# Kernel optimization log

Measured on AMD Instinct MI355X. Metric: run time of the kernel, lower is better.

Reference implementation:

```python
import jax, jax.numpy as jnp
import numpy as np

DIM = 96
NUM_HEADS = 3
WIN = 7  # window_size (square)


def _relative_position_index(wh, ww):
    coords = np.stack(np.meshgrid(np.arange(wh), np.arange(ww), indexing='ij'))  # [2, wh, ww]
    flat = coords.reshape(2, -1)  # [2, n]
    rel = flat[:, :, None] - flat[:, None, :]  # [2, n, n]
    rel = rel.transpose(1, 2, 0).astype(np.int64)
    rel[..., 0] += wh - 1
    rel[..., 1] += ww - 1
    rel[..., 0] *= 2 * ww - 1
    return rel.sum(-1)  # [n, n]


def setup_inputs() -> dict:
    key = jax.random.key(0)
    ks = jax.random.split(key, 9)
    b, n, c = 8192, WIN * WIN, DIM
    std = 0.02
    inp = {
        'x': jax.random.normal(ks[0], (b, n, c), jnp.float32),
        'v': jax.random.normal(ks[1], (b, n, c), jnp.float32),
        'w_q': jax.random.normal(ks[2], (c, c), jnp.float32) * std,
        'b_q': jnp.zeros((c,), jnp.float32),
        'w_kv': jax.random.normal(ks[3], (c, 2 * c), jnp.float32) * std,
        'b_kv': jnp.zeros((2 * c,), jnp.float32),
        'w_proj': jax.random.normal(ks[4], (c, c), jnp.float32) * std,
        'b_proj': jnp.zeros((c,), jnp.float32),
        'rpb_table': jax.random.normal(ks[5], ((2 * WIN - 1) * (2 * WIN - 1), NUM_HEADS), jnp.float32) * std,
        'rel_index': jnp.asarray(_relative_position_index(WIN, WIN), jnp.int32),
    }
    return inp


def reference(x, v, w_q, b_q, w_kv, b_kv, w_proj, b_proj, rpb_table, rel_index):
    b, n, c = x.shape
    h = NUM_HEADS
    hd = c // h
    scale = hd ** -0.5
    # q: [b, h, n, hd]
    q = (x @ w_q + b_q).reshape(b, n, h, hd).transpose(0, 2, 1, 3) * scale
    kv = (v @ w_kv + b_kv).reshape(b, n, 2, h, hd)
    k = kv[:, :, 0].transpose(0, 2, 1, 3)  # [b, h, n, hd]
    vv = kv[:, :, 1].transpose(0, 2, 1, 3)
    attn = jnp.einsum('bhqd,bhkd->bhqk', q, k)  # [b, h, n, n]
    bias = rpb_table[rel_index.reshape(-1)].reshape(n, n, h).transpose(2, 0, 1)  # [h, n, n]
    attn = jax.nn.softmax(attn + bias[None], axis=-1)
    out = jnp.einsum('bhqk,bhkd->bhqd', attn, vv).transpose(0, 2, 1, 3).reshape(b, n, c)
    return out @ w_proj + b_proj
```

## Files before the change

kernel.cpp:

```cpp
#include <hip/hip_runtime.h>
#include <hip/hip_bf16.h>

typedef __bf16 bf16x8 __attribute__((ext_vector_type(8)));
typedef float f32x4 __attribute__((ext_vector_type(4)));
typedef short s16x8 __attribute__((ext_vector_type(8)));
typedef short s16x4 __attribute__((ext_vector_type(4)));

#define NTOK 49
#define CDIM 96
#define KS_S 104
#define VT_S 56
#define BN_S 136
#define LOG2E 1.4426950408889634f

#if __has_builtin(__builtin_amdgcn_exp2f)
#define EXP2F(x) __builtin_amdgcn_exp2f(x)
#else
#define EXP2F(x) exp2f(x)
#endif

#define DRAIN() do { asm volatile("s_waitcnt lgkmcnt(0)" ::: "memory"); \
                     __builtin_amdgcn_sched_barrier(0); } while (0)

__device__ __forceinline__ unsigned short f2bf(float f) {
  __hip_bfloat16 h = __float2bfloat16(f);
  return __builtin_bit_cast(unsigned short, h);
}

__device__ __forceinline__ bf16x8 ld_cvt8(const float* p) {
  float4 a = *(const float4*)p;
  float4 b = *(const float4*)(p + 4);
  s16x8 r;
  r[0] = (short)f2bf(a.x); r[1] = (short)f2bf(a.y);
  r[2] = (short)f2bf(a.z); r[3] = (short)f2bf(a.w);
  r[4] = (short)f2bf(b.x); r[5] = (short)f2bf(b.y);
  r[6] = (short)f2bf(b.z); r[7] = (short)f2bf(b.w);
  return __builtin_bit_cast(bf16x8, r);
}

__global__ void prep(const float* __restrict__ wq, const float* __restrict__ wkv,
                     const float* __restrict__ wproj, const float* __restrict__ rpb,
                     const int* __restrict__ relidx, unsigned short* __restrict__ wsT,
                     float* __restrict__ biasf) {
  const int total = 36864 + 3 * 49 * 64;
  for (int i = blockIdx.x * 256 + threadIdx.x; i < total; i += gridDim.x * 256) {
    if (i < 9216) {
      int oc = i / 96, ic = i - oc * 96;
      wsT[i] = f2bf(wq[ic * 96 + oc]);
    } else if (i < 27648) {
      int j = i - 9216; int oc = j / 96, ic = j - oc * 96;
      wsT[i] = f2bf(wkv[ic * 192 + oc]);
    } else if (i < 36864) {
      int j = i - 27648; int oc = j / 96, ic = j - oc * 96;
      wsT[i] = f2bf(wproj[ic * 96 + oc]);
    } else {
      int j = i - 36864; int h = j / 3136; int rc = j - h * 3136;
      int r = rc >> 6, c = rc & 63;
      biasf[j] = (c < 49) ? rpb[relidx[r * 49 + c] * 3 + h] * LOG2E : 0.f;
    }
  }
}

__launch_bounds__(256, 4)
__global__ void attn_fused(const float* __restrict__ xg, const float* __restrict__ vg,
                           const float* __restrict__ bq, const float* __restrict__ bkv,
                           const float* __restrict__ bproj,
                           const unsigned short* __restrict__ wsT,
                           const float* __restrict__ biasf,
                           float* __restrict__ outg) {
  __shared__ __align__(16) unsigned char smem[38352];
  unsigned short* Ks  = (unsigned short*)smem;
  unsigned short* VVT = (unsigned short*)(smem + 10192);

  const int tid = threadIdx.x;
  const int lane = tid & 63;
  const int wv = tid >> 6;
  const int c16 = lane & 15;
  const int g4 = lane >> 4;
  const int win = blockIdx.x;
  const int q0 = (wv == 0) ? 0 : (wv == 1) ? 16 : (wv == 2) ? 32 : 33;
  unsigned short* bnc = (unsigned short*)(smem + 20944) + wv * (16 * BN_S);

  const int mp = wv & 1;
  const bool isK = (wv < 2);
  const int m0 = mp ? 32 : 0;
  const int m1 = mp ? 33 : 16;

  const float* base = xg + (size_t)win * (NTOK * CDIM);
  const float* vbase = vg + (size_t)win * (NTOK * CDIM);
  const float* xrow = base + (q0 + c16) * CDIM;
  const float* vrow0 = vbase + (m0 + c16) * CDIM;
  const float* vrow1 = vbase + (m1 + c16) * CDIM;

  bf16x8 xf[3], vf0[3], vf1[3];
#pragma unroll
  for (int k = 0; k < 3; ++k) {
    xf[k]  = ld_cvt8(xrow  + k * 32 + g4 * 8);
    vf0[k] = ld_cvt8(vrow0 + k * 32 + g4 * 8);
    vf1[k] = ld_cvt8(vrow1 + k * 32 + g4 * 8);
  }

  const float scale = 0.2550348742f;
#pragma unroll
  for (int nt = 0; nt < 6; ++nt) {
    f32x4 acc = {0, 0, 0, 0};
    const int ocl = nt * 16 + c16;
#pragma unroll
    for (int k = 0; k < 3; ++k) {
      bf16x8 b = *(const bf16x8*)(wsT + ocl * 96 + k * 32 + g4 * 8);
      acc = __builtin_amdgcn_mfma_f32_16x16x32_bf16(xf[k], b, acc, 0, 0, 0);
    }
    float bias = bq[ocl];
#pragma unroll
    for (int r = 0; r < 4; ++r)
      bnc[(4 * g4 + r) * BN_S + ocl] = f2bf((acc[r] + bias) * scale);
  }

#pragma unroll
  for (int nt = 0; nt < 6; ++nt) {
    const int ocl = (isK ? 0 : 96) + nt * 16 + c16;
    f32x4 a0 = {0, 0, 0, 0}, a1 = {0, 0, 0, 0};
#pragma unroll
    for (int k = 0; k < 3; ++k) {
      bf16x8 b = *(const bf16x8*)(wsT + 9216 + ocl * 96 + k * 32 + g4 * 8);
      a0 = __builtin_amdgcn_mfma_f32_16x16x32_bf16(vf0[k], b, a0, 0, 0, 0);
      a1 = __builtin_amdgcn_mfma_f32_16x16x32_bf16(vf1[k], b, a1, 0, 0, 0);
    }
    float bias = bkv[ocl];
    if (isK) {
#pragma unroll
      for (int r = 0; r < 4; ++r)
        Ks[(m0 + 4 * g4 + r) * KS_S + ocl] = f2bf(a0[r] + bias);
#pragma unroll
      for (int r = 0; r < 4; ++r)
        Ks[(m1 + 4 * g4 + r) * KS_S + ocl] = f2bf(a1[r] + bias);
    } else {
      int dim = ocl - 96;
      s16x4 p0;
#pragma unroll
      for (int r = 0; r < 4; ++r) p0[r] = (short)f2bf(a0[r] + bias);
      *(s16x4*)(VVT + dim * VT_S + (m0 + 4 * g4)) = p0;
      if (mp == 0) {
        s16x4 p1;
#pragma unroll
        for (int r = 0; r < 4; ++r) p1[r] = (short)f2bf(a1[r] + bias);
        *(s16x4*)(VVT + dim * VT_S + (16 + 4 * g4)) = p1;
      } else {
#pragma unroll
        for (int r = 0; r < 4; ++r)
          VVT[dim * VT_S + 33 + 4 * g4 + r] = f2bf(a1[r] + bias);
      }
    }
  }
  __syncthreads();

  const int q = q0 + c16;

  s16x8 vmask;
#pragma unroll
  for (int j = 0; j < 8; ++j)
    vmask[j] = (short)(((32 + g4 * 8 + j) < 49) ? 0xFFFF : 0x0000);

  f32x4 oacc[6] = {{0,0,0,0},{0,0,0,0},{0,0,0,0},{0,0,0,0},{0,0,0,0},{0,0,0,0}};

  auto softmax_pw = [&](const f32x4* s, const f32x4* bv, int pcol) {
    float vals[16];
#pragma unroll
    for (int kt = 0; kt < 4; ++kt)
#pragma unroll
      for (int r = 0; r < 4; ++r) {
        int key = 16 * kt + 4 * g4 + r;
        vals[kt * 4 + r] = (kt < 3 || key < 49) ? (s[kt][r] + bv[kt][r]) : -1e30f;
      }
    float m8[8];
#pragma unroll
    for (int j = 0; j < 8; ++j) m8[j] = fmaxf(vals[j], vals[j + 8]);
    float ma = fmaxf(m8[0], m8[4]), mb = fmaxf(m8[1], m8[5]);
    float mc = fmaxf(m8[2], m8[6]), md = fmaxf(m8[3], m8[7]);
    float mx = fmaxf(fmaxf(ma, mb), fmaxf(mc, md));
    mx = fmaxf(mx, __shfl_xor(mx, 16, 64));
    mx = fmaxf(mx, __shfl_xor(mx, 32, 64));
    float e[16];
#pragma unroll
    for (int j = 0; j < 16; ++j) e[j] = EXP2F(vals[j] - mx);
    float s8[8];
#pragma unroll
    for (int j = 0; j < 8; ++j) s8[j] = e[j] + e[j + 8];
    float sa = s8[0] + s8[4], sb = s8[1] + s8[5], sc = s8[2] + s8[6], sd = s8[3] + s8[7];
    float sum = (sa + sb) + (sc + sd);
    sum += __shfl_xor(sum, 16, 64);
    sum += __shfl_xor(sum, 32, 64);
    float rinv = 1.0f / sum;
#pragma unroll
    for (int kt = 0; kt < 4; ++kt) {
      s16x4 p;
#pragma unroll
      for (int r = 0; r < 4; ++r) p[r] = (short)f2bf(e[kt * 4 + r] * rinv);
      *(s16x4*)(bnc + c16 * BN_S + pcol + 16 * kt + 4 * g4) = p;
    }
  };

  auto pv_out = [&](int h, int pcol, int ocol) {
    bf16x8 ap0 = *(const bf16x8*)(bnc + c16 * BN_S + pcol + g4 * 8);
    bf16x8 ap1 = *(const bf16x8*)(bnc + c16 * BN_S + pcol + 32 + g4 * 8);
#pragma unroll
    for (int dt = 0; dt < 2; ++dt) {
      int dim = h * 32 + dt * 16 + c16;
      bf16x8 bv0 = *(const bf16x8*)(VVT + dim * VT_S + g4 * 8);
      s16x8 b1 = *(const s16x8*)(VVT + dim * VT_S + 32 + g4 * 8);
      b1 &= vmask;
      f32x4 o = __builtin_amdgcn_mfma_f32_16x16x32_bf16(ap0, bv0, (f32x4){0,0,0,0}, 0, 0, 0);
      o = __builtin_amdgcn_mfma_f32_16x16x32_bf16(ap1, __builtin_bit_cast(bf16x8, b1), o, 0, 0, 0);
#pragma unroll
      for (int r = 0; r < 4; ++r)
        bnc[(4 * g4 + r) * BN_S + ocol + dt * 16 + c16] = f2bf(o[r]);
    }
  };

  auto oproj = [&](int h, int ocol) {
    bf16x8 bo = *(const bf16x8*)(bnc + c16 * BN_S + ocol + g4 * 8);
#pragma unroll
    for (int mt = 0; mt < 6; ++mt) {
      bf16x8 a = *(const bf16x8*)(wsT + 27648 + (mt * 16 + c16) * 96 + h * 32 + g4 * 8);
      oacc[mt] = __builtin_amdgcn_mfma_f32_16x16x32_bf16(a, bo, oacc[mt], 0, 0, 0);
    }
  };

  f32x4 b0v[4], b1v[4];
  {
    const float* br0 = biasf + q * 64 + 4 * g4;
    const float* br1 = biasf + (49 + q) * 64 + 4 * g4;
#pragma unroll
    for (int kt = 0; kt < 4; ++kt) {
      b0v[kt] = *(const f32x4*)(br0 + 16 * kt);
      b1v[kt] = *(const f32x4*)(br1 + 16 * kt);
    }
  }
  bf16x8 qf0 = *(const bf16x8*)(bnc + c16 * BN_S + g4 * 8);
  bf16x8 qf1 = *(const bf16x8*)(bnc + c16 * BN_S + 32 + g4 * 8);
  bf16x8 qf2 = *(const bf16x8*)(bnc + c16 * BN_S + 64 + g4 * 8);

  f32x4 s0[4], s1[4];
#pragma unroll
  for (int kt = 0; kt < 4; ++kt) {
    bf16x8 ak = *(const bf16x8*)(Ks + (16 * kt + c16) * KS_S + g4 * 8);
    s0[kt] = __builtin_amdgcn_mfma_f32_16x16x32_bf16(ak, qf0, (f32x4){0,0,0,0}, 0, 0, 0);
  }
#pragma unroll
  for (int kt = 0; kt < 4; ++kt) {
    bf16x8 ak = *(const bf16x8*)(Ks + (16 * kt + c16) * KS_S + 32 + g4 * 8);
    s1[kt] = __builtin_amdgcn_mfma_f32_16x16x32_bf16(ak, qf1, (f32x4){0,0,0,0}, 0, 0, 0);
  }
  softmax_pw(s0, b0v, 0);
  softmax_pw(s1, b1v, 64);

  f32x4 b2v[4];
  {
    const float* br2 = biasf + (98 + q) * 64 + 4 * g4;
#pragma unroll
    for (int kt = 0; kt < 4; ++kt) b2v[kt] = *(const f32x4*)(br2 + 16 * kt);
  }
  f32x4 s2[4];
#pragma unroll
  for (int kt = 0; kt < 4; ++kt) {
    bf16x8 ak = *(const bf16x8*)(Ks + (16 * kt + c16) * KS_S + 64 + g4 * 8);
    s2[kt] = __builtin_amdgcn_mfma_f32_16x16x32_bf16(ak, qf2, (f32x4){0,0,0,0}, 0, 0, 0);
  }

  DRAIN();
  pv_out(0, 0, 0);
  pv_out(1, 64, 32);
  softmax_pw(s2, b2v, 64);

  DRAIN();
  oproj(0, 0);
  oproj(1, 32);
  pv_out(2, 64, 96);

  DRAIN();
  oproj(2, 96);

  {
    const bool store_ok = (wv < 3) || (c16 == 15);
    float* orow = outg + (size_t)win * (NTOK * CDIM) + q * 96;
#pragma unroll
    for (int mt = 0; mt < 6; ++mt) {
      int oc0 = mt * 16 + g4 * 4;
      if (store_ok) {
        float4 bb = *(const float4*)(bproj + oc0);
        float4 o4;
        o4.x = oacc[mt][0] + bb.x; o4.y = oacc[mt][1] + bb.y;
        o4.z = oacc[mt][2] + bb.z; o4.w = oacc[mt][3] + bb.w;
        *(float4*)(orow + oc0) = o4;
      }
    }
  }
}

extern "C" void kernel_launch(void* const* d_in, const int* in_sizes, int n_in,
                              void* d_out, int out_size, void* d_ws, size_t ws_size,
                              hipStream_t stream) {
  const float* x     = (const float*)d_in[0];
  const float* v     = (const float*)d_in[1];
  const float* wq    = (const float*)d_in[2];
  const float* bq    = (const float*)d_in[3];
  const float* wkv   = (const float*)d_in[4];
  const float* bkv   = (const float*)d_in[5];
  const float* wproj = (const float*)d_in[6];
  const float* bproj = (const float*)d_in[7];
  const float* rpb   = (const float*)d_in[8];
  const int*   relidx= (const int*)d_in[9];
  float* out = (float*)d_out;
  unsigned short* wsT = (unsigned short*)d_ws;
  float* biasf = (float*)((char*)d_ws + 73728);
  int nwin = in_sizes[0] / (NTOK * CDIM);

  hipLaunchKernelGGL(prep, dim3(181), dim3(256), 0, stream,
                     wq, wkv, wproj, rpb, relidx, wsT, biasf);
  hipLaunchKernelGGL(attn_fused, dim3(nwin), dim3(256), 0, stream,
                     x, v, bq, bkv, bproj, wsT, biasf, out);
}
```

Measured before the change: 251.0 us.

## Split fused attention into K/V projection kernel and attention kernel via workspace

Adds a proj_kv kernel that computes K and transposed V in bf16 and writes them to a global workspace. A second kernel, attn2, computes Q and then reads K and V^T straight from global memory to do softmax, PV and the output projection. Both new kernels use far less shared memory and declare 8 blocks per CU, and attn2 needs no block-wide barrier. The aim is higher occupancy and better latency hiding, paid for with about 165 MB of extra global write and read traffic. The old fused kernel remains as a fallback when the workspace is too small.

```diff
diff --git a/kernel.cpp b/kernel.cpp
--- a/kernel.cpp
+++ b/kernel.cpp
@@ -11,7 +11,12 @@
 #define KS_S 104
 #define VT_S 56
 #define BN_S 136
+#define PB_S 104
 #define LOG2E 1.4426950408889634f
+
+#define WS_K_B 111616
+#define WS_VT_B 77181952
+#define WS_NEED 165262400ull
 
 #if __has_builtin(__builtin_amdgcn_exp2f)
 #define EXP2F(x) __builtin_amdgcn_exp2f(x)
@@ -61,6 +66,254 @@
   }
 }
 
+__launch_bounds__(256, 8)
+__global__ void proj_kv(const float* __restrict__ vg, const float* __restrict__ bkv,
+                        const unsigned short* __restrict__ wsT,
+                        unsigned short* __restrict__ kbuf,
+                        unsigned short* __restrict__ vtbuf) {
+  __shared__ __align__(16) unsigned short bnc_all[4 * 16 * PB_S];
+  const int tid = threadIdx.x, lane = tid & 63, wv = tid >> 6;
+  const int c16 = lane & 15, g4 = lane >> 4;
+  const int win = blockIdx.x;
+  const int q0 = (wv == 0) ? 0 : (wv == 1) ? 16 : (wv == 2) ? 32 : 33;
+  unsigned short* bnc = bnc_all + wv * (16 * PB_S);
+
+  const float* vrow = vg + (size_t)win * (NTOK * CDIM) + (q0 + c16) * CDIM;
+  bf16x8 vf[3];
+#pragma unroll
+  for (int k = 0; k < 3; ++k) vf[k] = ld_cvt8(vrow + k * 32 + g4 * 8);
+
+#pragma unroll
+  for (int nt = 0; nt < 6; ++nt) {
+    const int ocl = 96 + nt * 16 + c16;
+    f32x4 acc = {0, 0, 0, 0};
+#pragma unroll
+    for (int k = 0; k < 3; ++k) {
+      bf16x8 b = *(const bf16x8*)(wsT + 9216 + ocl * 96 + k * 32 + g4 * 8);
+      acc = __builtin_amdgcn_mfma_f32_16x16x32_bf16(vf[k], b, acc, 0, 0, 0);
+    }
+    float bias = bkv[ocl];
+    const int dim = nt * 16 + c16;
+    const int rb = q0 + 4 * g4;
+    unsigned short* vtr = vtbuf + ((size_t)win * CDIM + dim) * VT_S;
+    if (wv < 3) {
+      s16x4 p;
+#pragma unroll
+      for (int r = 0; r < 4; ++r) p[r] = (short)f2bf(acc[r] + bias);
+      *(s16x4*)(vtr + rb) = p;
+    } else {
+#pragma unroll
+      for (int r = 0; r < 4; ++r) vtr[rb + r] = f2bf(acc[r] + bias);
+    }
+  }
+
+#pragma unroll
+  for (int nt = 0; nt < 6; ++nt) {
+    const int ocl = nt * 16 + c16;
+    f32x4 acc = {0, 0, 0, 0};
+#pragma unroll
+    for (int k = 0; k < 3; ++k) {
+      bf16x8 b = *(const bf16x8*)(wsT + 9216 + ocl * 96 + k * 32 + g4 * 8);
+      acc = __builtin_amdgcn_mfma_f32_16x16x32_bf16(vf[k], b, acc, 0, 0, 0);
+    }
+    float bias = bkv[ocl];
+#pragma unroll
+    for (int r = 0; r < 4; ++r)
+      bnc[(4 * g4 + r) * PB_S + ocl] = f2bf(acc[r] + bias);
+  }
+  DRAIN();
+  const bool store_ok = (wv < 3) || (c16 == 15);
+  if (store_ok) {
+    unsigned short* krow = kbuf + ((size_t)win * NTOK + q0 + c16) * CDIM;
+#pragma unroll
+    for (int kk = 0; kk < 3; ++kk) {
+      s16x8 t = *(const s16x8*)(bnc + c16 * PB_S + kk * 32 + g4 * 8);
+      *(s16x8*)(krow + kk * 32 + g4 * 8) = t;
+    }
+  }
+}
+
+__launch_bounds__(256, 8)
+__global__ void attn2(const float* __restrict__ xg, const float* __restrict__ bq,
+                      const float* __restrict__ bproj,
+                      const unsigned short* __restrict__ wsT,
+                      const float* __restrict__ biasf,
+                      const unsigned short* __restrict__ kbuf,
+                      const unsigned short* __restrict__ vtbuf,
+                      float* __restrict__ outg) {
+  __shared__ __align__(16) unsigned short bnc_all[4 * 16 * BN_S];
+  const int tid = threadIdx.x, lane = tid & 63, wv = tid >> 6;
+  const int c16 = lane & 15, g4 = lane >> 4;
+  const int win = blockIdx.x;
+  const int q0 = (wv == 0) ? 0 : (wv == 1) ? 16 : (wv == 2) ? 32 : 33;
+  unsigned short* bnc = bnc_all + wv * (16 * BN_S);
+
+  const float* xrow = xg + (size_t)win * (NTOK * CDIM) + (q0 + c16) * CDIM;
+  const unsigned short* kw = kbuf + (size_t)win * (NTOK * CDIM);
+  const unsigned short* vtw = vtbuf + (size_t)win * (CDIM * VT_S);
+
+  bf16x8 xf[3];
+#pragma unroll
+  for (int k = 0; k < 3; ++k) xf[k] = ld_cvt8(xrow + k * 32 + g4 * 8);
+  const float scale = 0.2550348742f;
+#pragma unroll
+  for (int nt = 0; nt < 6; ++nt) {
+    f32x4 acc = {0, 0, 0, 0};
+    const int ocl = nt * 16 + c16;
+#pragma unroll
+    for (int k = 0; k < 3; ++k) {
+      bf16x8 b = *(const bf16x8*)(wsT + ocl * 96 + k * 32 + g4 * 8);
+      acc = __builtin_amdgcn_mfma_f32_16x16x32_bf16(xf[k], b, acc, 0, 0, 0);
+    }
+    float bias = bq[ocl];
+#pragma unroll
+    for (int r = 0; r < 4; ++r)
+      bnc[(4 * g4 + r) * BN_S + ocl] = f2bf((acc[r] + bias) * scale);
+  }
+  DRAIN();
+
+  const int q = q0 + c16;
+  s16x8 vmask;
+#pragma unroll
+  for (int j = 0; j < 8; ++j)
+    vmask[j] = (short)(((32 + g4 * 8 + j) < 49) ? 0xFFFF : 0x0000);
+
+  f32x4 oacc[6] = {{0,0,0,0},{0,0,0,0},{0,0,0,0},{0,0,0,0},{0,0,0,0},{0,0,0,0}};
+
+  auto softmax_pw = [&](const f32x4* s, const f32x4* bv, int pcol) {
+    float vals[16];
+#pragma unroll
+    for (int kt = 0; kt < 4; ++kt)
+#pragma unroll
+      for (int r = 0; r < 4; ++r) {
+        int key = 16 * kt + 4 * g4 + r;
+        vals[kt * 4 + r] = (kt < 3 || key < 49) ? (s[kt][r] + bv[kt][r]) : -1e30f;
+      }
+    float m8[8];
+#pragma unroll
+    for (int j = 0; j < 8; ++j) m8[j] = fmaxf(vals[j], vals[j + 8]);
+    float ma = fmaxf(m8[0], m8[4]), mb = fmaxf(m8[1], m8[5]);
+    float mc = fmaxf(m8[2], m8[6]), md = fmaxf(m8[3], m8[7]);
+    float mx = fmaxf(fmaxf(ma, mb), fmaxf(mc, md));
+    mx = fmaxf(mx, __shfl_xor(mx, 16, 64));
+    mx = fmaxf(mx, __shfl_xor(mx, 32, 64));
+    float e[16];
+#pragma unroll
+    for (int j = 0; j < 16; ++j) e[j] = EXP2F(vals[j] - mx);
+    float s8[8];
+#pragma unroll
+    for (int j = 0; j < 8; ++j) s8[j] = e[j] + e[j + 8];
+    float sa = s8[0] + s8[4], sb = s8[1] + s8[5], sc = s8[2] + s8[6], sd = s8[3] + s8[7];
+    float sum = (sa + sb) + (sc + sd);
+    sum += __shfl_xor(sum, 16, 64);
+    sum += __shfl_xor(sum, 32, 64);
+    float rinv = 1.0f / sum;
+#pragma unroll
+    for (int kt = 0; kt < 4; ++kt) {
+      s16x4 p;
+#pragma unroll
+      for (int r = 0; r < 4; ++r) p[r] = (short)f2bf(e[kt * 4 + r] * rinv);
+      *(s16x4*)(bnc + c16 * BN_S + pcol + 16 * kt + 4 * g4) = p;
+    }
+  };
+
+  auto pv_out = [&](int h, int pcol, int ocol) {
+    bf16x8 ap0 = *(const bf16x8*)(bnc + c16 * BN_S + pcol + g4 * 8);
+    bf16x8 ap1 = *(const bf16x8*)(bnc + c16 * BN_S + pcol + 32 + g4 * 8);
+#pragma unroll
+    for (int dt = 0; dt < 2; ++dt) {
+      int dim = h * 32 + dt * 16 + c16;
+      bf16x8 bv0 = *(const bf16x8*)(vtw + dim * VT_S + g4 * 8);
+      s16x8 b1 = *(const s16x8*)(vtw + dim * VT_S + 32 + g4 * 8);
+      b1 &= vmask;
+      f32x4 o = __builtin_amdgcn_mfma_f32_16x16x32_bf16(ap0, bv0, (f32x4){0,0,0,0}, 0, 0, 0);
+      o = __builtin_amdgcn_mfma_f32_16x16x32_bf16(ap1, __builtin_bit_cast(bf16x8, b1), o, 0, 0, 0);
+#pragma unroll
+      for (int r = 0; r < 4; ++r)
+        bnc[(4 * g4 + r) * BN_S + ocol + dt * 16 + c16] = f2bf(o[r]);
+    }
+  };
+
+  auto oproj = [&](int h, int ocol) {
+    bf16x8 bo = *(const bf16x8*)(bnc + c16 * BN_S + ocol + g4 * 8);
+#pragma unroll
+    for (int mt = 0; mt < 6; ++mt) {
+      bf16x8 a = *(const bf16x8*)(wsT + 27648 + (mt * 16 + c16) * 96 + h * 32 + g4 * 8);
+      oacc[mt] = __builtin_amdgcn_mfma_f32_16x16x32_bf16(a, bo, oacc[mt], 0, 0, 0);
+    }
+  };
+
+  f32x4 b0v[4], b1v[4];
+  {
+    const float* br0 = biasf + q * 64 + 4 * g4;
+    const float* br1 = biasf + (49 + q) * 64 + 4 * g4;
+#pragma unroll
+    for (int kt = 0; kt < 4; ++kt) {
+      b0v[kt] = *(const f32x4*)(br0 + 16 * kt);
+      b1v[kt] = *(const f32x4*)(br1 + 16 * kt);
+    }
+  }
+  bf16x8 qf0 = *(const bf16x8*)(bnc + c16 * BN_S + g4 * 8);
+  bf16x8 qf1 = *(const bf16x8*)(bnc + c16 * BN_S + 32 + g4 * 8);
+  bf16x8 qf2 = *(const bf16x8*)(bnc + c16 * BN_S + 64 + g4 * 8);
+
+  f32x4 s0[4], s1[4];
+#pragma unroll
+  for (int kt = 0; kt < 4; ++kt) {
+    bf16x8 ak = *(const bf16x8*)(kw + (16 * kt + c16) * CDIM + g4 * 8);
+    s0[kt] = __builtin_amdgcn_mfma_f32_16x16x32_bf16(ak, qf0, (f32x4){0,0,0,0}, 0, 0, 0);
+  }
+#pragma unroll
+  for (int kt = 0; kt < 4; ++kt) {
+    bf16x8 ak = *(const bf16x8*)(kw + (16 * kt + c16) * CDIM + 32 + g4 * 8);
+    s1[kt] = __builtin_amdgcn_mfma_f32_16x16x32_bf16(ak, qf1, (f32x4){0,0,0,0}, 0, 0, 0);
+  }
+  softmax_pw(s0, b0v, 0);
+  softmax_pw(s1, b1v, 64);
+
+  f32x4 b2v[4];
+  {
+    const float* br2 = biasf + (98 + q) * 64 + 4 * g4;
+#pragma unroll
+    for (int kt = 0; kt < 4; ++kt) b2v[kt] = *(const f32x4*)(br2 + 16 * kt);
+  }
+  f32x4 s2[4];
+#pragma unroll
+  for (int kt = 0; kt < 4; ++kt) {
+    bf16x8 ak = *(const bf16x8*)(kw + (16 * kt + c16) * CDIM + 64 + g4 * 8);
+    s2[kt] = __builtin_amdgcn_mfma_f32_16x16x32_bf16(ak, qf2, (f32x4){0,0,0,0}, 0, 0, 0);
+  }
+
+  DRAIN();
+  pv_out(0, 0, 0);
+  pv_out(1, 64, 32);
+  softmax_pw(s2, b2v, 64);
+
+  DRAIN();
+  oproj(0, 0);
+  oproj(1, 32);
+  pv_out(2, 64, 96);
+
+  DRAIN();
+  oproj(2, 96);
+
+  {
+    const bool store_ok = (wv < 3) || (c16 == 15);
+    float* orow = outg + (size_t)win * (NTOK * CDIM) + q * 96;
+#pragma unroll
+    for (int mt = 0; mt < 6; ++mt) {
+      int oc0 = mt * 16 + g4 * 4;
+      if (store_ok) {
+        float4 bb = *(const float4*)(bproj + oc0);
+        float4 o4;
+        o4.x = oacc[mt][0] + bb.x; o4.y = oacc[mt][1] + bb.y;
+        o4.z = oacc[mt][2] + bb.z; o4.w = oacc[mt][3] + bb.w;
+        *(float4*)(orow + oc0) = o4;
+      }
+    }
+  }
+}
+
 __launch_bounds__(256, 4)
 __global__ void attn_fused(const float* __restrict__ xg, const float* __restrict__ vg,
                            const float* __restrict__ bq, const float* __restrict__ bkv,
@@ -71,27 +324,20 @@
   __shared__ __align__(16) unsigned char smem[38352];
   unsigned short* Ks  = (unsigned short*)smem;
   unsigned short* VVT = (unsigned short*)(smem + 10192);
-
-  const int tid = threadIdx.x;
-  const int lane = tid & 63;
-  const int wv = tid >> 6;
-  const int c16 = lane & 15;
-  const int g4 = lane >> 4;
+  const int tid = threadIdx.x, lane = tid & 63, wv = tid >> 6;
+  const int c16 = lane & 15, g4 = lane >> 4;
   const int win = blockIdx.x;
   const int q0 = (wv == 0) ? 0 : (wv == 1) ? 16 : (wv == 2) ? 32 : 33;
   unsigned short* bnc = (unsigned short*)(smem + 20944) + wv * (16 * BN_S);
-
   const int mp = wv & 1;
   const bool isK = (wv < 2);
   const int m0 = mp ? 32 : 0;
   const int m1 = mp ? 33 : 16;
-
   const float* base = xg + (size_t)win * (NTOK * CDIM);
   const float* vbase = vg + (size_t)win * (NTOK * CDIM);
   const float* xrow = base + (q0 + c16) * CDIM;
   const float* vrow0 = vbase + (m0 + c16) * CDIM;
   const float* vrow1 = vbase + (m1 + c16) * CDIM;
-
   bf16x8 xf[3], vf0[3], vf1[3];
 #pragma unroll
   for (int k = 0; k < 3; ++k) {
@@ -99,7 +345,6 @@
     vf0[k] = ld_cvt8(vrow0 + k * 32 + g4 * 8);
     vf1[k] = ld_cvt8(vrow1 + k * 32 + g4 * 8);
   }
-
   const float scale = 0.2550348742f;
 #pragma unroll
   for (int nt = 0; nt < 6; ++nt) {
@@ -115,7 +360,6 @@
     for (int r = 0; r < 4; ++r)
       bnc[(4 * g4 + r) * BN_S + ocl] = f2bf((acc[r] + bias) * scale);
   }
-
 #pragma unroll
   for (int nt = 0; nt < 6; ++nt) {
     const int ocl = (isK ? 0 : 96) + nt * 16 + c16;
@@ -129,11 +373,9 @@
     float bias = bkv[ocl];
     if (isK) {
 #pragma unroll
-      for (int r = 0; r < 4; ++r)
-        Ks[(m0 + 4 * g4 + r) * KS_S + ocl] = f2bf(a0[r] + bias);
-#pragma unroll
-      for (int r = 0; r < 4; ++r)
-        Ks[(m1 + 4 * g4 + r) * KS_S + ocl] = f2bf(a1[r] + bias);
+      for (int r = 0; r < 4; ++r) Ks[(m0 + 4 * g4 + r) * KS_S + ocl] = f2bf(a0[r] + bias);
+#pragma unroll
+      for (int r = 0; r < 4; ++r) Ks[(m1 + 4 * g4 + r) * KS_S + ocl] = f2bf(a1[r] + bias);
     } else {
       int dim = ocl - 96;
       s16x4 p0;
@@ -147,22 +389,17 @@
         *(s16x4*)(VVT + dim * VT_S + (16 + 4 * g4)) = p1;
       } else {
 #pragma unroll
-        for (int r = 0; r < 4; ++r)
-          VVT[dim * VT_S + 33 + 4 * g4 + r] = f2bf(a1[r] + bias);
+        for (int r = 0; r < 4; ++r) VVT[dim * VT_S + 33 + 4 * g4 + r] = f2bf(a1[r] + bias);
       }
     }
   }
   __syncthreads();
-
   const int q = q0 + c16;
-
   s16x8 vmask;
 #pragma unroll
   for (int j = 0; j < 8; ++j)
     vmask[j] = (short)(((32 + g4 * 8 + j) < 49) ? 0xFFFF : 0x0000);
-
   f32x4 oacc[6] = {{0,0,0,0},{0,0,0,0},{0,0,0,0},{0,0,0,0},{0,0,0,0},{0,0,0,0}};
-
   auto softmax_pw = [&](const f32x4* s, const f32x4* bv, int pcol) {
     float vals[16];
 #pragma unroll
@@ -199,7 +436,6 @@
       *(s16x4*)(bnc + c16 * BN_S + pcol + 16 * kt + 4 * g4) = p;
     }
   };
-
   auto pv_out = [&](int h, int pcol, int ocol) {
     bf16x8 ap0 = *(const bf16x8*)(bnc + c16 * BN_S + pcol + g4 * 8);
     bf16x8 ap1 = *(const bf16x8*)(bnc + c16 * BN_S + pcol + 32 + g4 * 8);
@@ -216,7 +452,6 @@
         bnc[(4 * g4 + r) * BN_S + ocol + dt * 16 + c16] = f2bf(o[r]);
     }
   };
-
   auto oproj = [&](int h, int ocol) {
     bf16x8 bo = *(const bf16x8*)(bnc + c16 * BN_S + ocol + g4 * 8);
 #pragma unroll
@@ -225,7 +460,6 @@
       oacc[mt] = __builtin_amdgcn_mfma_f32_16x16x32_bf16(a, bo, oacc[mt], 0, 0, 0);
     }
   };
-
   f32x4 b0v[4], b1v[4];
   {
     const float* br0 = biasf + q * 64 + 4 * g4;
@@ -239,7 +473,6 @@
   bf16x8 qf0 = *(const bf16x8*)(bnc + c16 * BN_S + g4 * 8);
   bf16x8 qf1 = *(const bf16x8*)(bnc + c16 * BN_S + 32 + g4 * 8);
   bf16x8 qf2 = *(const bf16x8*)(bnc + c16 * BN_S + 64 + g4 * 8);
-
   f32x4 s0[4], s1[4];
 #pragma unroll
   for (int kt = 0; kt < 4; ++kt) {
@@ -253,7 +486,6 @@
   }
   softmax_pw(s0, b0v, 0);
   softmax_pw(s1, b1v, 64);
-
   f32x4 b2v[4];
   {
     const float* br2 = biasf + (98 + q) * 64 + 4 * g4;
@@ -266,20 +498,16 @@
     bf16x8 ak = *(const bf16x8*)(Ks + (16 * kt + c16) * KS_S + 64 + g4 * 8);
     s2[kt] = __builtin_amdgcn_mfma_f32_16x16x32_bf16(ak, qf2, (f32x4){0,0,0,0}, 0, 0, 0);
   }
-
   DRAIN();
   pv_out(0, 0, 0);
   pv_out(1, 64, 32);
   softmax_pw(s2, b2v, 64);
-
   DRAIN();
   oproj(0, 0);
   oproj(1, 32);
   pv_out(2, 64, 96);
-
   DRAIN();
   oproj(2, 96);
-
   {
     const bool store_ok = (wv < 3) || (c16 == 15);
     float* orow = outg + (size_t)win * (NTOK * CDIM) + q * 96;
@@ -317,6 +545,16 @@
 
   hipLaunchKernelGGL(prep, dim3(181), dim3(256), 0, stream,
                      wq, wkv, wproj, rpb, relidx, wsT, biasf);
-  hipLaunchKernelGGL(attn_fused, dim3(nwin), dim3(256), 0, stream,
-                     x, v, bq, bkv, bproj, wsT, biasf, out);
-}
+
+  if (ws_size >= (size_t)WS_NEED) {
+    unsigned short* kbuf  = (unsigned short*)((char*)d_ws + WS_K_B);
+    unsigned short* vtbuf = (unsigned short*)((char*)d_ws + WS_VT_B);
+    hipLaunchKernelGGL(proj_kv, dim3(nwin), dim3(256), 0, stream,
+                       v, bkv, wsT, kbuf, vtbuf);
+    hipLaunchKernelGGL(attn2, dim3(nwin), dim3(256), 0, stream,
+                       x, bq, bproj, wsT, biasf, kbuf, vtbuf, out);
+  } else {
+    hipLaunchKernelGGL(attn_fused, dim3(nwin), dim3(256), 0, stream,
+                       x, v, bq, bkv, bproj, wsT, biasf, out);
+  }
+}
```

Result: slower. 408.3 us (+62.7%).

## Make attention kernel persistent with register prefetch of next window inputs

Applied to the files above, without the earlier changes.

Replaces the one-block-per-window launch with a fixed grid of 768 persistent blocks that loop over windows. Each block loads the next window's x and v rows into registers right after the first barrier, so global loads overlap the attention and projection compute of the current window. This costs extra registers (launch bounds drop to 3 blocks per SM) and adds a second barrier per iteration, which may reduce occupancy-based latency hiding.

```diff
diff --git a/kernel.cpp b/kernel.cpp
--- a/kernel.cpp
+++ b/kernel.cpp
@@ -11,6 +11,7 @@
 #define KS_S 104
 #define VT_S 56
 #define BN_S 136
+#define GRID 768
 #define LOG2E 1.4426950408889634f
 
 #if __has_builtin(__builtin_amdgcn_exp2f)
@@ -27,9 +28,7 @@
   return __builtin_bit_cast(unsigned short, h);
 }
 
-__device__ __forceinline__ bf16x8 ld_cvt8(const float* p) {
-  float4 a = *(const float4*)p;
-  float4 b = *(const float4*)(p + 4);
+__device__ __forceinline__ bf16x8 cvt8(float4 a, float4 b) {
   s16x8 r;
   r[0] = (short)f2bf(a.x); r[1] = (short)f2bf(a.y);
   r[2] = (short)f2bf(a.z); r[3] = (short)f2bf(a.w);
@@ -61,23 +60,19 @@
   }
 }
 
-__launch_bounds__(256, 4)
-__global__ void attn_fused(const float* __restrict__ xg, const float* __restrict__ vg,
-                           const float* __restrict__ bq, const float* __restrict__ bkv,
-                           const float* __restrict__ bproj,
-                           const unsigned short* __restrict__ wsT,
-                           const float* __restrict__ biasf,
-                           float* __restrict__ outg) {
+__launch_bounds__(256, 3)
+__global__ void attn_persist(const float* __restrict__ xg, const float* __restrict__ vg,
+                             const float* __restrict__ bq, const float* __restrict__ bkv,
+                             const float* __restrict__ bproj,
+                             const unsigned short* __restrict__ wsT,
+                             const float* __restrict__ biasf,
+                             float* __restrict__ outg, int nwin) {
   __shared__ __align__(16) unsigned char smem[38352];
   unsigned short* Ks  = (unsigned short*)smem;
   unsigned short* VVT = (unsigned short*)(smem + 10192);
 
-  const int tid = threadIdx.x;
-  const int lane = tid & 63;
-  const int wv = tid >> 6;
-  const int c16 = lane & 15;
-  const int g4 = lane >> 4;
-  const int win = blockIdx.x;
+  const int tid = threadIdx.x, lane = tid & 63, wv = tid >> 6;
+  const int c16 = lane & 15, g4 = lane >> 4;
   const int q0 = (wv == 0) ? 0 : (wv == 1) ? 16 : (wv == 2) ? 32 : 33;
   unsigned short* bnc = (unsigned short*)(smem + 20944) + wv * (16 * BN_S);
 
@@ -86,214 +81,238 @@
   const int m0 = mp ? 32 : 0;
   const int m1 = mp ? 33 : 16;
 
-  const float* base = xg + (size_t)win * (NTOK * CDIM);
-  const float* vbase = vg + (size_t)win * (NTOK * CDIM);
-  const float* xrow = base + (q0 + c16) * CDIM;
-  const float* vrow0 = vbase + (m0 + c16) * CDIM;
-  const float* vrow1 = vbase + (m1 + c16) * CDIM;
-
-  bf16x8 xf[3], vf0[3], vf1[3];
-#pragma unroll
-  for (int k = 0; k < 3; ++k) {
-    xf[k]  = ld_cvt8(xrow  + k * 32 + g4 * 8);
-    vf0[k] = ld_cvt8(vrow0 + k * 32 + g4 * 8);
-    vf1[k] = ld_cvt8(vrow1 + k * 32 + g4 * 8);
-  }
-
-  const float scale = 0.2550348742f;
-#pragma unroll
-  for (int nt = 0; nt < 6; ++nt) {
-    f32x4 acc = {0, 0, 0, 0};
-    const int ocl = nt * 16 + c16;
-#pragma unroll
-    for (int k = 0; k < 3; ++k) {
-      bf16x8 b = *(const bf16x8*)(wsT + ocl * 96 + k * 32 + g4 * 8);
-      acc = __builtin_amdgcn_mfma_f32_16x16x32_bf16(xf[k], b, acc, 0, 0, 0);
-    }
-    float bias = bq[ocl];
-#pragma unroll
-    for (int r = 0; r < 4; ++r)
-      bnc[(4 * g4 + r) * BN_S + ocl] = f2bf((acc[r] + bias) * scale);
-  }
-
-#pragma unroll
-  for (int nt = 0; nt < 6; ++nt) {
-    const int ocl = (isK ? 0 : 96) + nt * 16 + c16;
-    f32x4 a0 = {0, 0, 0, 0}, a1 = {0, 0, 0, 0};
-#pragma unroll
-    for (int k = 0; k < 3; ++k) {
-      bf16x8 b = *(const bf16x8*)(wsT + 9216 + ocl * 96 + k * 32 + g4 * 8);
-      a0 = __builtin_amdgcn_mfma_f32_16x16x32_bf16(vf0[k], b, a0, 0, 0, 0);
-      a1 = __builtin_amdgcn_mfma_f32_16x16x32_bf16(vf1[k], b, a1, 0, 0, 0);
-    }
-    float bias = bkv[ocl];
-    if (isK) {
-#pragma unroll
-      for (int r = 0; r < 4; ++r)
-        Ks[(m0 + 4 * g4 + r) * KS_S + ocl] = f2bf(a0[r] + bias);
-#pragma unroll
-      for (int r = 0; r < 4; ++r)
-        Ks[(m1 + 4 * g4 + r) * KS_S + ocl] = f2bf(a1[r] + bias);
-    } else {
-      int dim = ocl - 96;
-      s16x4 p0;
-#pragma unroll
-      for (int r = 0; r < 4; ++r) p0[r] = (short)f2bf(a0[r] + bias);
-      *(s16x4*)(VVT + dim * VT_S + (m0 + 4 * g4)) = p0;
-      if (mp == 0) {
-        s16x4 p1;
-#pragma unroll
-        for (int r = 0; r < 4; ++r) p1[r] = (short)f2bf(a1[r] + bias);
-        *(s16x4*)(VVT + dim * VT_S + (16 + 4 * g4)) = p1;
-      } else {
-#pragma unroll
-        for (int r = 0; r < 4; ++r)
-          VVT[dim * VT_S + 33 + 4 * g4 + r] = f2bf(a1[r] + bias);
-      }
-    }
-  }
-  __syncthreads();
+  const size_t WSTRIDE = NTOK * CDIM;
+  const float* xq  = xg + (size_t)(q0 + c16) * CDIM;
+  const float* vq0 = vg + (size_t)(m0 + c16) * CDIM;
+  const float* vq1 = vg + (size_t)(m1 + c16) * CDIM;
 
   const int q = q0 + c16;
-
+  const bool store_ok = (wv < 3) || (c16 == 15);
   s16x8 vmask;
 #pragma unroll
   for (int j = 0; j < 8; ++j)
     vmask[j] = (short)(((32 + g4 * 8 + j) < 49) ? 0xFFFF : 0x0000);
 
-  f32x4 oacc[6] = {{0,0,0,0},{0,0,0,0},{0,0,0,0},{0,0,0,0},{0,0,0,0},{0,0,0,0}};
-
-  auto softmax_pw = [&](const f32x4* s, const f32x4* bv, int pcol) {
-    float vals[16];
-#pragma unroll
-    for (int kt = 0; kt < 4; ++kt)
-#pragma unroll
-      for (int r = 0; r < 4; ++r) {
-        int key = 16 * kt + 4 * g4 + r;
-        vals[kt * 4 + r] = (kt < 3 || key < 49) ? (s[kt][r] + bv[kt][r]) : -1e30f;
-      }
-    float m8[8];
-#pragma unroll
-    for (int j = 0; j < 8; ++j) m8[j] = fmaxf(vals[j], vals[j + 8]);
-    float ma = fmaxf(m8[0], m8[4]), mb = fmaxf(m8[1], m8[5]);
-    float mc = fmaxf(m8[2], m8[6]), md = fmaxf(m8[3], m8[7]);
-    float mx = fmaxf(fmaxf(ma, mb), fmaxf(mc, md));
-    mx = fmaxf(mx, __shfl_xor(mx, 16, 64));
-    mx = fmaxf(mx, __shfl_xor(mx, 32, 64));
-    float e[16];
-#pragma unroll
-    for (int j = 0; j < 16; ++j) e[j] = EXP2F(vals[j] - mx);
-    float s8[8];
-#pragma unroll
-    for (int j = 0; j < 8; ++j) s8[j] = e[j] + e[j + 8];
-    float sa = s8[0] + s8[4], sb = s8[1] + s8[5], sc = s8[2] + s8[6], sd = s8[3] + s8[7];
-    float sum = (sa + sb) + (sc + sd);
-    sum += __shfl_xor(sum, 16, 64);
-    sum += __shfl_xor(sum, 32, 64);
-    float rinv = 1.0f / sum;
+  const float scale = 0.2550348742f;
+
+  float4 px[6], pv0[6], pv1[6];
+  auto prefetch = [&](int w) {
+    const float* xr = xq  + (size_t)w * WSTRIDE;
+    const float* v0 = vq0 + (size_t)w * WSTRIDE;
+    const float* v1 = vq1 + (size_t)w * WSTRIDE;
+#pragma unroll
+    for (int k = 0; k < 3; ++k) {
+      const int off = k * 32 + g4 * 8;
+      px[2*k]    = *(const float4*)(xr + off);
+      px[2*k+1]  = *(const float4*)(xr + off + 4);
+      pv0[2*k]   = *(const float4*)(v0 + off);
+      pv0[2*k+1] = *(const float4*)(v0 + off + 4);
+      pv1[2*k]   = *(const float4*)(v1 + off);
+      pv1[2*k+1] = *(const float4*)(v1 + off + 4);
+    }
+  };
+
+  int win = blockIdx.x;
+  if (win < nwin) prefetch(win);
+
+  for (; win < nwin; win += GRID) {
+    bf16x8 xf[3], vf0[3], vf1[3];
+#pragma unroll
+    for (int k = 0; k < 3; ++k) {
+      xf[k]  = cvt8(px[2*k],  px[2*k+1]);
+      vf0[k] = cvt8(pv0[2*k], pv0[2*k+1]);
+      vf1[k] = cvt8(pv1[2*k], pv1[2*k+1]);
+    }
+
+#pragma unroll
+    for (int nt = 0; nt < 6; ++nt) {
+      f32x4 acc = {0, 0, 0, 0};
+      const int ocl = nt * 16 + c16;
+#pragma unroll
+      for (int k = 0; k < 3; ++k) {
+        bf16x8 b = *(const bf16x8*)(wsT + ocl * 96 + k * 32 + g4 * 8);
+        acc = __builtin_amdgcn_mfma_f32_16x16x32_bf16(xf[k], b, acc, 0, 0, 0);
+      }
+      float bias = bq[ocl];
+#pragma unroll
+      for (int r = 0; r < 4; ++r)
+        bnc[(4 * g4 + r) * BN_S + ocl] = f2bf((acc[r] + bias) * scale);
+    }
+
+#pragma unroll
+    for (int nt = 0; nt < 6; ++nt) {
+      const int ocl = (isK ? 0 : 96) + nt * 16 + c16;
+      f32x4 a0 = {0, 0, 0, 0}, a1 = {0, 0, 0, 0};
+#pragma unroll
+      for (int k = 0; k < 3; ++k) {
+        bf16x8 b = *(const bf16x8*)(wsT + 9216 + ocl * 96 + k * 32 + g4 * 8);
+        a0 = __builtin_amdgcn_mfma_f32_16x16x32_bf16(vf0[k], b, a0, 0, 0, 0);
+        a1 = __builtin_amdgcn_mfma_f32_16x16x32_bf16(vf1[k], b, a1, 0, 0, 0);
+      }
+      float bias = bkv[ocl];
+      if (isK) {
+#pragma unroll
+        for (int r = 0; r < 4; ++r)
+          Ks[(m0 + 4 * g4 + r) * KS_S + ocl] = f2bf(a0[r] + bias);
+#pragma unroll
+        for (int r = 0; r < 4; ++r)
+          Ks[(m1 + 4 * g4 + r) * KS_S + ocl] = f2bf(a1[r] + bias);
+      } else {
+        int dim = ocl - 96;
+        s16x4 p0;
+#pragma unroll
+        for (int r = 0; r < 4; ++r) p0[r] = (short)f2bf(a0[r] + bias);
+        *(s16x4*)(VVT + dim * VT_S + (m0 + 4 * g4)) = p0;
+        if (mp == 0) {
+          s16x4 p1;
+#pragma unroll
+          for (int r = 0; r < 4; ++r) p1[r] = (short)f2bf(a1[r] + bias);
+          *(s16x4*)(VVT + dim * VT_S + (16 + 4 * g4)) = p1;
+        } else {
+#pragma unroll
+          for (int r = 0; r < 4; ++r)
+            VVT[dim * VT_S + 33 + 4 * g4 + r] = f2bf(a1[r] + bias);
+        }
+      }
+    }
+    __syncthreads();
+
+    if (win + GRID < nwin) prefetch(win + GRID);
+
+    f32x4 oacc[6] = {{0,0,0,0},{0,0,0,0},{0,0,0,0},{0,0,0,0},{0,0,0,0},{0,0,0,0}};
+
+    auto softmax_pw = [&](const f32x4* s, const f32x4* bv, int pcol) {
+      float vals[16];
+#pragma unroll
+      for (int kt = 0; kt < 4; ++kt)
+#pragma unroll
+        for (int r = 0; r < 4; ++r) {
+          int key = 16 * kt + 4 * g4 + r;
+          vals[kt * 4 + r] = (kt < 3 || key < 49) ? (s[kt][r] + bv[kt][r]) : -1e30f;
+        }
+      float m8[8];
+#pragma unroll
+      for (int j = 0; j < 8; ++j) m8[j] = fmaxf(vals[j], vals[j + 8]);
+      float ma = fmaxf(m8[0], m8[4]), mb = fmaxf(m8[1], m8[5]);
+      float mc = fmaxf(m8[2], m8[6]), md = fmaxf(m8[3], m8[7]);
+      float mx = fmaxf(fmaxf(ma, mb), fmaxf(mc, md));
+      mx = fmaxf(mx, __shfl_xor(mx, 16, 64));
+      mx = fmaxf(mx, __shfl_xor(mx, 32, 64));
+      float e[16];
+#pragma unroll
+      for (int j = 0; j < 16; ++j) e[j] = EXP2F(vals[j] - mx);
+      float s8[8];
+#pragma unroll
+      for (int j = 0; j < 8; ++j) s8[j] = e[j] + e[j + 8];
+      float sa = s8[0] + s8[4], sb = s8[1] + s8[5], sc = s8[2] + s8[6], sd = s8[3] + s8[7];
+      float sum = (sa + sb) + (sc + sd);
+      sum += __shfl_xor(sum, 16, 64);
+      sum += __shfl_xor(sum, 32, 64);
+      float rinv = 1.0f / sum;
+#pragma unroll
+      for (int kt = 0; kt < 4; ++kt) {
+        s16x4 p;
+#pragma unroll
+        for (int r = 0; r < 4; ++r) p[r] = (short)f2bf(e[kt * 4 + r] * rinv);
+        *(s16x4*)(bnc + c16 * BN_S + pcol + 16 * kt + 4 * g4) = p;
+      }
+    };
+
+    auto pv_out = [&](int h, int pcol, int ocol) {
+      bf16x8 ap0 = *(const bf16x8*)(bnc + c16 * BN_S + pcol + g4 * 8);
+      bf16x8 ap1 = *(const bf16x8*)(bnc + c16 * BN_S + pcol + 32 + g4 * 8);
+#pragma unroll
+      for (int dt = 0; dt < 2; ++dt) {
+        int dim = h * 32 + dt * 16 + c16;
+        bf16x8 bv0 = *(const bf16x8*)(VVT + dim * VT_S + g4 * 8);
+        s16x8 b1 = *(const s16x8*)(VVT + dim * VT_S + 32 + g4 * 8);
+        b1 &= vmask;
+        f32x4 o = __builtin_amdgcn_mfma_f32_16x16x32_bf16(ap0, bv0, (f32x4){0,0,0,0}, 0, 0, 0);
+        o = __builtin_amdgcn_mfma_f32_16x16x32_bf16(ap1, __builtin_bit_cast(bf16x8, b1), o, 0, 0, 0);
+#pragma unroll
+        for (int r = 0; r < 4; ++r)
+          bnc[(4 * g4 + r) * BN_S + ocol + dt * 16 + c16] = f2bf(o[r]);
+      }
+    };
+
+    auto oproj = [&](int h, int ocol) {
+      bf16x8 bo = *(const bf16x8*)(bnc + c16 * BN_S + ocol + g4 * 8);
+#pragma unroll
+      for (int mt = 0; mt < 6; ++mt) {
+        bf16x8 a = *(const bf16x8*)(wsT + 27648 + (mt * 16 + c16) * 96 + h * 32 + g4 * 8);
+        oacc[mt] = __builtin_amdgcn_mfma_f32_16x16x32_bf16(a, bo, oacc[mt], 0, 0, 0);
+      }
+    };
+
+    f32x4 b0v[4], b1v[4];
+    {
+      const float* br0 = biasf + q * 64 + 4 * g4;
+      const float* br1 = biasf + (49 + q) * 64 + 4 * g4;
+#pragma unroll
+      for (int kt = 0; kt < 4; ++kt) {
+        b0v[kt] = *(const f32x4*)(br0 + 16 * kt);
+        b1v[kt] = *(const f32x4*)(br1 + 16 * kt);
+      }
+    }
+    bf16x8 qf0 = *(const bf16x8*)(bnc + c16 * BN_S + g4 * 8);
+    bf16x8 qf1 = *(const bf16x8*)(bnc + c16 * BN_S + 32 + g4 * 8);
+    bf16x8 qf2 = *(const bf16x8*)(bnc + c16 * BN_S + 64 + g4 * 8);
+
+    f32x4 s0[4], s1[4];
 #pragma unroll
     for (int kt = 0; kt < 4; ++kt) {
-      s16x4 p;
-#pragma unroll
-      for (int r = 0; r < 4; ++r) p[r] = (short)f2bf(e[kt * 4 + r] * rinv);
-      *(s16x4*)(bnc + c16 * BN_S + pcol + 16 * kt + 4 * g4) = p;
-    }
-  };
-
-  auto pv_out = [&](int h, int pcol, int ocol) {
-    bf16x8 ap0 = *(const bf16x8*)(bnc + c16 * BN_S + pcol + g4 * 8);
-    bf16x8 ap1 = *(const bf16x8*)(bnc + c16 * BN_S + pcol + 32 + g4 * 8);
-#pragma unroll
-    for (int dt = 0; dt < 2; ++dt) {
-      int dim = h * 32 + dt * 16 + c16;
-      bf16x8 bv0 = *(const bf16x8*)(VVT + dim * VT_S + g4 * 8);
-      s16x8 b1 = *(const s16x8*)(VVT + dim * VT_S + 32 + g4 * 8);
-      b1 &= vmask;
-      f32x4 o = __builtin_amdgcn_mfma_f32_16x16x32_bf16(ap0, bv0, (f32x4){0,0,0,0}, 0, 0, 0);
-      o = __builtin_amdgcn_mfma_f32_16x16x32_bf16(ap1, __builtin_bit_cast(bf16x8, b1), o, 0, 0, 0);
-#pragma unroll
-      for (int r = 0; r < 4; ++r)
-        bnc[(4 * g4 + r) * BN_S + ocol + dt * 16 + c16] = f2bf(o[r]);
-    }
-  };
-
-  auto oproj = [&](int h, int ocol) {
-    bf16x8 bo = *(const bf16x8*)(bnc + c16 * BN_S + ocol + g4 * 8);
-#pragma unroll
-    for (int mt = 0; mt < 6; ++mt) {
-      bf16x8 a = *(const bf16x8*)(wsT + 27648 + (mt * 16 + c16) * 96 + h * 32 + g4 * 8);
-      oacc[mt] = __builtin_amdgcn_mfma_f32_16x16x32_bf16(a, bo, oacc[mt], 0, 0, 0);
-    }
-  };
-
-  f32x4 b0v[4], b1v[4];
-  {
-    const float* br0 = biasf + q * 64 + 4 * g4;
-    const float* br1 = biasf + (49 + q) * 64 + 4 * g4;
+      bf16x8 ak = *(const bf16x8*)(Ks + (16 * kt + c16) * KS_S + g4 * 8);
+      s0[kt] = __builtin_amdgcn_mfma_f32_16x16x32_bf16(ak, qf0, (f32x4){0,0,0,0}, 0, 0, 0);
+    }
 #pragma unroll
     for (int kt = 0; kt < 4; ++kt) {
-      b0v[kt] = *(const f32x4*)(br0 + 16 * kt);
-      b1v[kt] = *(const f32x4*)(br1 + 16 * kt);
-    }
-  }
-  bf16x8 qf0 = *(const bf16x8*)(bnc + c16 * BN_S + g4 * 8);
-  bf16x8 qf1 = *(const bf16x8*)(bnc + c16 * BN_S + 32 + g4 * 8);
-  bf16x8 qf2 = *(const bf16x8*)(bnc + c16 * BN_S + 64 + g4 * 8);
-
-  f32x4 s0[4], s1[4];
-#pragma unroll
-  for (int kt = 0; kt < 4; ++kt) {
-    bf16x8 ak = *(const bf16x8*)(Ks + (16 * kt + c16) * KS_S + g4 * 8);
-    s0[kt] = __builtin_amdgcn_mfma_f32_16x16x32_bf16(ak, qf0, (f32x4){0,0,0,0}, 0, 0, 0);
-  }
-#pragma unroll
-  for (int kt = 0; kt < 4; ++kt) {
-    bf16x8 ak = *(const bf16x8*)(Ks + (16 * kt + c16) * KS_S + 32 + g4 * 8);
-    s1[kt] = __builtin_amdgcn_mfma_f32_16x16x32_bf16(ak, qf1, (f32x4){0,0,0,0}, 0, 0, 0);
-  }
-  softmax_pw(s0, b0v, 0);
-  softmax_pw(s1, b1v, 64);
-
-  f32x4 b2v[4];
-  {
-    const float* br2 = biasf + (98 + q) * 64 + 4 * g4;
-#pragma unroll
-    for (int kt = 0; kt < 4; ++kt) b2v[kt] = *(const f32x4*)(br2 + 16 * kt);
-  }
-  f32x4 s2[4];
-#pragma unroll
-  for (int kt = 0; kt < 4; ++kt) {
-    bf16x8 ak = *(const bf16x8*)(Ks + (16 * kt + c16) * KS_S + 64 + g4 * 8);
-    s2[kt] = __builtin_amdgcn_mfma_f32_16x16x32_bf16(ak, qf2, (f32x4){0,0,0,0}, 0, 0, 0);
-  }
-
-  DRAIN();
-  pv_out(0, 0, 0);
-  pv_out(1, 64, 32);
-  softmax_pw(s2, b2v, 64);
-
-  DRAIN();
-  oproj(0, 0);
-  oproj(1, 32);
-  pv_out(2, 64, 96);
-
-  DRAIN();
-  oproj(2, 96);
-
-  {
-    const bool store_ok = (wv < 3) || (c16 == 15);
-    float* orow = outg + (size_t)win * (NTOK * CDIM) + q * 96;
-#pragma unroll
-    for (int mt = 0; mt < 6; ++mt) {
-      int oc0 = mt * 16 + g4 * 4;
-      if (store_ok) {
-        float4 bb = *(const float4*)(bproj + oc0);
-        float4 o4;
-        o4.x = oacc[mt][0] + bb.x; o4.y = oacc[mt][1] + bb.y;
-        o4.z = oacc[mt][2] + bb.z; o4.w = oacc[mt][3] + bb.w;
-        *(float4*)(orow + oc0) = o4;
-      }
-    }
+      bf16x8 ak = *(const bf16x8*)(Ks + (16 * kt + c16) * KS_S + 32 + g4 * 8);
+      s1[kt] = __builtin_amdgcn_mfma_f32_16x16x32_bf16(ak, qf1, (f32x4){0,0,0,0}, 0, 0, 0);
+    }
+    softmax_pw(s0, b0v, 0);
+    softmax_pw(s1, b1v, 64);
+
+    f32x4 b2v[4];
+    {
+      const float* br2 = biasf + (98 + q) * 64 + 4 * g4;
+#pragma unroll
+      for (int kt = 0; kt < 4; ++kt) b2v[kt] = *(const f32x4*)(br2 + 16 * kt);
+    }
+    f32x4 s2[4];
+#pragma unroll
+    for (int kt = 0; kt < 4; ++kt) {
+      bf16x8 ak = *(const bf16x8*)(Ks + (16 * kt + c16) * KS_S + 64 + g4 * 8);
+      s2[kt] = __builtin_amdgcn_mfma_f32_16x16x32_bf16(ak, qf2, (f32x4){0,0,0,0}, 0, 0, 0);
+    }
+
+    DRAIN();
+    pv_out(0, 0, 0);
+    pv_out(1, 64, 32);
+    softmax_pw(s2, b2v, 64);
+
+    DRAIN();
+    oproj(0, 0);
+    oproj(1, 32);
+    pv_out(2, 64, 96);
+
+    DRAIN();
+    oproj(2, 96);
+
+    {
+      float* orow = outg + (size_t)win * WSTRIDE + q * 96;
+#pragma unroll
+      for (int mt = 0; mt < 6; ++mt) {
+        int oc0 = mt * 16 + g4 * 4;
+        if (store_ok) {
+          float4 bb = *(const float4*)(bproj + oc0);
+          float4 o4;
+          o4.x = oacc[mt][0] + bb.x; o4.y = oacc[mt][1] + bb.y;
+          o4.z = oacc[mt][2] + bb.z; o4.w = oacc[mt][3] + bb.w;
+          *(float4*)(orow + oc0) = o4;
+        }
+      }
+    }
+    __syncthreads();
   }
 }
 
@@ -317,6 +336,6 @@
 
   hipLaunchKernelGGL(prep, dim3(181), dim3(256), 0, stream,
                      wq, wkv, wproj, rpb, relidx, wsT, biasf);
-  hipLaunchKernelGGL(attn_fused, dim3(nwin), dim3(256), 0, stream,
-                     x, v, bq, bkv, bproj, wsT, biasf, out);
-}
+  hipLaunchKernelGGL(attn_persist, dim3(GRID), dim3(256), 0, stream,
+                     x, v, bq, bkv, bproj, wsT, biasf, out, nwin);
+}
```

Result: slower. 626.4 us (+149.5%).
